# Kernel tuning notes

Hardware: AMD Instinct MI355X
Metric: run time of the kernel (lower is better)

The kernel has to match this reference:

```python
import jax, jax.numpy as jnp
import numpy as np

STEP_SIZE = 0.3333
MAX_STEPS = 8          # >= ceil(max(2*sigma)/step); extra iterations have k==0 (no-op)
TANGENT_DIRECTION = True


def _bilinear_sample(img, p):
    # img: [B,C,H,W], p: [B,2,H,W] normalized coords in [0,1] (x=width, y=height)
    B, C, H, W = img.shape
    fx = p[:, 0] * W - 0.5   # [B,H,W] pixel-center convention
    fy = p[:, 1] * H - 0.5
    x0 = jnp.floor(fx)
    y0 = jnp.floor(fy)
    wx = (fx - x0)[:, None]  # [B,1,H,W]
    wy = (fy - y0)[:, None]
    x0i = jnp.clip(x0.astype(jnp.int32), 0, W - 1)
    x1i = jnp.clip(x0i + 1, 0, W - 1)
    y0i = jnp.clip(y0.astype(jnp.int32), 0, H - 1)
    y1i = jnp.clip(y0i + 1, 0, H - 1)
    gather = jax.vmap(lambda im, yi, xi: im[:, yi, xi])  # per-batch gather -> [B,C,H,W]
    v00 = gather(img, y0i, x0i)
    v01 = gather(img, y0i, x1i)
    v10 = gather(img, y1i, x0i)
    v11 = gather(img, y1i, x1i)
    return (v00 * (1 - wx) + v01 * wx) * (1 - wy) + (v10 * (1 - wx) + v11 * wx) * wy


def _p_start(H, W, dtype):
    xs = (jnp.arange(W, dtype=dtype) + 0.5) / W
    ys = (jnp.arange(H, dtype=dtype) + 0.5) / H
    px = jnp.broadcast_to(xs[None, :], (H, W))
    py = jnp.broadcast_to(ys[:, None], (H, W))
    return jnp.stack([px, py])[None]  # [1,2,H,W]


def _perp(t):
    return jnp.concatenate([t[:, 1:2], -t[:, 0:1]], axis=1)


def _forward(x, tangent, sigma):
    B, C, H, W = x.shape
    dt = x.dtype
    factor = min(H, W) / 1024.0          # input_size_factor relative to 1024 base res
    sigma = sigma * factor               # [B,1,1,1]
    half_width = 2.0 * sigma
    two_sigma2 = 2.0 * sigma * sigma
    step = jnp.asarray(1.0 / (STEP_SIZE * factor), dtype=dt)
    tex = jnp.array([W, H], dtype=dt).reshape(1, 2, 1, 1)
    p0 = _p_start(H, W, dt)

    def one_pass(direction):
        v = direction if TANGENT_DIRECTION else _perp(direction)
        p = p0 + v / tex
        r = jnp.broadcast_to(step, (B, 1, 1, 1))
        c = jnp.zeros_like(x)
        s = jnp.zeros((B, 1, H, W), dt)

        def body(carry, _):
            c, s, v, p, r = carry
            k = jnp.exp(-r * r / two_sigma2)                 # [B,1,1,1]
            k = jnp.where(r < half_width, k, 0.0)
            inb = ((p[:, 0:1] >= 0.0) & (p[:, 0:1] < 1.0) &
                   (p[:, 1:2] >= 0.0) & (p[:, 1:2] < 1.0))   # [B,1,H,W]
            k = jnp.where(inb, k, 0.0)                        # [B,1,H,W]
            c = c + _bilinear_sample(x, p) * k
            s = s + k
            tf = _bilinear_sample(tangent, p)                 # [B,2,H,W]
            if not TANGENT_DIRECTION:
                tf = _perp(tf)
            vt = jnp.sum(v * tf, axis=1, keepdims=True)
            tf = jnp.where(vt < 0.0, -tf, tf)                 # keep marching direction coherent
            return (c, s, tf, p + tf / tex, r + step), None

        (c, s, _, _, _), _ = jax.lax.scan(body, (c, s, v, p, r), None, length=MAX_STEPS)
        return c, s

    c1, s1 = one_pass(tangent)
    c2, s2 = one_pass(-tangent)
    return (x + c1 + c2) / (1.0 + s1 + s2)


def setup_inputs() -> dict:
    key = jax.random.key(0)
    k1, k2, k3 = jax.random.split(key, 3)
    B, C, H, W = 2, 3, 1024, 1024
    x = jax.random.uniform(k1, (B, C, H, W), dtype=jnp.float32)
    t = jax.random.normal(k2, (B, 2, H, W), dtype=jnp.float32)
    t = t / (jnp.sqrt(jnp.sum(t * t, axis=1, keepdims=True)) + 1e-6)  # unit tangent field
    sigma = 2.0 + 4.0 * jax.random.uniform(k3, (B, 1, 1, 1), dtype=jnp.float32)
    return {"x": x, "tangent": t, "sigma": sigma}


def reference(x, tangent, sigma):
    return _forward(x, tangent, sigma)
```

## Files before the change

### kernel.cpp

```cpp
#include <hip/hip_runtime.h>


#define HH 1024
#define WW 1024
#define CC 3
#define BB 2
#define NPIX (HH * WW)

#define TSX 16
#define TSY 16
#define HALO_LO 5
#define NWIN 27

__device__ __forceinline__ unsigned bf16rn(float f) {
    unsigned u = __float_as_uint(f);
    unsigned r = u + 0x7fffu + ((u >> 16) & 1u);
    return r >> 16;
}
__device__ __forceinline__ float bf_lo(unsigned u) { return __uint_as_float(u << 16); }
__device__ __forceinline__ float bf_hi(unsigned u) { return __uint_as_float(u & 0xffff0000u); }

__global__ __launch_bounds__(256) void flow_smooth_lds(
    const float* __restrict__ x, const float* __restrict__ tng,
    const float* __restrict__ sigma, float* __restrict__ out)
{
    __shared__ uint4 win[NWIN * NWIN];

    const int b = blockIdx.z;
    const int tile_x0 = blockIdx.x * TSX;
    const int tile_y0 = blockIdx.y * TSY;
    const int win_x0 = tile_x0 - HALO_LO;
    const int win_y0 = tile_y0 - HALO_LO;

    const float* __restrict__ xb  = x   + (size_t)b * CC * NPIX;
    const float* __restrict__ tbx = tng + (size_t)b * 2 * NPIX;
    const float* __restrict__ tby = tbx + NPIX;

    for (int j = threadIdx.x; j < NWIN * NWIN; j += 256) {
        const int jy = j / NWIN;
        const int jx = j - jy * NWIN;
        const int gy = min(max(win_y0 + jy, 0), HH - 1);
        const int gx = min(max(win_x0 + jx, 0), WW - 1);
        const int g  = gy * WW + gx;
        uint4 rec;
        rec.x = __float_as_uint(tbx[g]);
        rec.y = __float_as_uint(tby[g]);
        rec.z = bf16rn(xb[g]) | (bf16rn(xb[NPIX + g]) << 16);
        rec.w = bf16rn(xb[2 * NPIX + g]);
        win[j] = rec;
    }
    __syncthreads();

    const int ix = tile_x0 + (threadIdx.x & (TSX - 1));
    const int iy = tile_y0 + (threadIdx.x >> 4);
    const int pix = iy * WW + ix;

    const float sig = sigma[b];
    const float half_width = 2.0f * sig;
    const float inv_two_sigma2 = 1.0f / (2.0f * sig * sig);
    const float step = (float)(1.0 / 0.3333);

    const float xc0 = xb[pix];
    const float xc1 = xb[NPIX + pix];
    const float xc2 = xb[2 * NPIX + pix];
    const float t0x = tbx[pix];
    const float t0y = tby[pix];

    const float invW = 1.0f / WW;
    const float invH = 1.0f / HH;

    float acc0 = 0.f, acc1 = 0.f, acc2 = 0.f, accs = 0.f;

    float vx[2], vy[2], px[2], py[2];
    vx[0] = t0x;  vy[0] = t0y;
    vx[1] = -t0x; vy[1] = -t0y;
    const float p0x = ((float)ix + 0.5f) * invW;
    const float p0y = ((float)iy + 0.5f) * invH;
    px[0] = p0x + vx[0] * invW;  py[0] = p0y + vy[0] * invH;
    px[1] = p0x + vx[1] * invW;  py[1] = p0y + vy[1] * invH;

    float r = step;
    for (int it = 0; it < 8; ++it) {
        if (!(r < half_width)) break;
        const float k = __expf(-r * r * inv_two_sigma2);

        #pragma unroll
        for (int c = 0; c < 2; ++c) {
            const float fx = px[c] * (float)WW - 0.5f;
            const float fy = py[c] * (float)HH - 0.5f;
            const float x0f = floorf(fx);
            const float y0f = floorf(fy);
            const float wx = fx - x0f;
            const float wy = fy - y0f;
            int x0i = (int)x0f;
            int y0i = (int)y0f;
            x0i = min(max(x0i, 0), WW - 1);
            y0i = min(max(y0i, 0), HH - 1);
            const int x1i = min(x0i + 1, WW - 1);
            const int y1i = min(y0i + 1, HH - 1);

            const int jx0 = x0i - win_x0;
            const int jx1 = x1i - win_x0;
            const int jy0 = y0i - win_y0;
            const int jy1 = y1i - win_y0;

            const uint4 q00 = win[jy0 * NWIN + jx0];
            const uint4 q01 = win[jy0 * NWIN + jx1];
            const uint4 q10 = win[jy1 * NWIN + jx0];
            const uint4 q11 = win[jy1 * NWIN + jx1];

            const float wxm = 1.f - wx;
            const float wym = 1.f - wy;
            const float w00 = wxm * wym, w01 = wx * wym;
            const float w10 = wxm * wy,  w11 = wx * wy;

            float tfx = __uint_as_float(q00.x) * w00 + __uint_as_float(q01.x) * w01
                      + __uint_as_float(q10.x) * w10 + __uint_as_float(q11.x) * w11;
            float tfy = __uint_as_float(q00.y) * w00 + __uint_as_float(q01.y) * w01
                      + __uint_as_float(q10.y) * w10 + __uint_as_float(q11.y) * w11;

            const bool inb = (px[c] >= 0.f) && (px[c] < 1.f) &&
                             (py[c] >= 0.f) && (py[c] < 1.f);
            if (inb) {
                acc0 += k * (bf_lo(q00.z) * w00 + bf_lo(q01.z) * w01 +
                             bf_lo(q10.z) * w10 + bf_lo(q11.z) * w11);
                acc1 += k * (bf_hi(q00.z) * w00 + bf_hi(q01.z) * w01 +
                             bf_hi(q10.z) * w10 + bf_hi(q11.z) * w11);
                acc2 += k * (bf_lo(q00.w) * w00 + bf_lo(q01.w) * w01 +
                             bf_lo(q10.w) * w10 + bf_lo(q11.w) * w11);
                accs += k;
            }

            const float vt = vx[c] * tfx + vy[c] * tfy;
            if (vt < 0.f) { tfx = -tfx; tfy = -tfy; }
            vx[c] = tfx; vy[c] = tfy;
            px[c] += tfx * invW;
            py[c] += tfy * invH;
        }
        r += step;
    }

    const float inv_den = 1.0f / (1.0f + accs);
    float* ob = out + (size_t)b * CC * NPIX;
    ob[pix]            = (xc0 + acc0) * inv_den;
    ob[NPIX + pix]     = (xc1 + acc1) * inv_den;
    ob[2 * NPIX + pix] = (xc2 + acc2) * inv_den;
}

extern "C" void kernel_launch(void* const* d_in, const int* in_sizes, int n_in,
                              void* d_out, int out_size, void* d_ws, size_t ws_size,
                              hipStream_t stream) {
    const float* x  = (const float*)d_in[0];
    const float* t  = (const float*)d_in[1];
    const float* sg = (const float*)d_in[2];
    float* out = (float*)d_out;

    dim3 grid(WW / TSX, HH / TSY, BB);
    flow_smooth_lds<<<grid, dim3(256), 0, stream>>>(x, t, sg, out);
}
```

Before: 118.7 us.

## Use 32x32 tiles with four pixels per thread and a clamp-free interior path

Result: slower. 123.0 us (+3.6%).

```diff
diff --git a/kernel.cpp b/kernel.cpp
--- a/kernel.cpp
+++ b/kernel.cpp
@@ -1,4 +1,5 @@
 #include <hip/hip_runtime.h>
+#include <hip/hip_fp16.h>
 
 
 #define HH 1024
@@ -7,28 +8,119 @@
 #define BB 2
 #define NPIX (HH * WW)
 
-#define TSX 16
-#define TSY 16
+#define TS 32
 #define HALO_LO 5
-#define NWIN 27
-
-__device__ __forceinline__ unsigned bf16rn(float f) {
-    unsigned u = __float_as_uint(f);
-    unsigned r = u + 0x7fffu + ((u >> 16) & 1u);
-    return r >> 16;
-}
-__device__ __forceinline__ float bf_lo(unsigned u) { return __uint_as_float(u << 16); }
-__device__ __forceinline__ float bf_hi(unsigned u) { return __uint_as_float(u & 0xffff0000u); }
-
-__global__ __launch_bounds__(256) void flow_smooth_lds(
+#define NWIN 43
+#define NREC (NWIN * NWIN)
+
+__device__ __forceinline__ unsigned pk_f16x2(float a, float b) {
+    __half2 h = __floats2half2_rn(a, b);
+    return *(const unsigned*)&h;
+}
+__device__ __forceinline__ float2 unpk_f16x2(unsigned u) {
+    __half2 h = *(const __half2*)&u;
+    return __half22float2(h);
+}
+
+template <bool BORDER>
+__device__ __forceinline__ float4 march_pixel(
+    const uint4* __restrict__ win, int win_x0, int win_y0,
+    int ix, int iy, float t0x, float t0y,
+    float half_width, float inv_two_sigma2, float step)
+{
+    const float invT = 1.0f / 1024.0f;
+    float acc0 = 0.f, acc1 = 0.f, acc2 = 0.f, accs = 0.f;
+
+    float vx[2], vy[2], px[2], py[2];
+    vx[0] = t0x;  vy[0] = t0y;
+    vx[1] = -t0x; vy[1] = -t0y;
+    const float p0x = ((float)ix + 0.5f) * invT;
+    const float p0y = ((float)iy + 0.5f) * invT;
+    px[0] = p0x + vx[0] * invT;  py[0] = p0y + vy[0] * invT;
+    px[1] = p0x + vx[1] * invT;  py[1] = p0y + vy[1] * invT;
+
+    float r = step;
+    for (int it = 0; it < 8; ++it) {
+        if (!(r < half_width)) break;
+        const float k = __expf(-r * r * inv_two_sigma2);
+
+        #pragma unroll
+        for (int c = 0; c < 2; ++c) {
+            const float fx = px[c] * 1024.0f - 0.5f;
+            const float fy = py[c] * 1024.0f - 0.5f;
+            const float x0f = floorf(fx);
+            const float y0f = floorf(fy);
+            const float wx = fx - x0f;
+            const float wy = fy - y0f;
+
+            int jx0, jx1, jy0, jy1;
+            if (BORDER) {
+                int x0i = (int)x0f, y0i = (int)y0f;
+                x0i = min(max(x0i, 0), WW - 1);
+                y0i = min(max(y0i, 0), HH - 1);
+                const int x1i = min(x0i + 1, WW - 1);
+                const int y1i = min(y0i + 1, HH - 1);
+                jx0 = x0i - win_x0; jx1 = x1i - win_x0;
+                jy0 = y0i - win_y0; jy1 = y1i - win_y0;
+            } else {
+                jx0 = (int)x0f - win_x0; jx1 = jx0 + 1;
+                jy0 = (int)y0f - win_y0; jy1 = jy0 + 1;
+            }
+
+            const uint4 q00 = win[jy0 * NWIN + jx0];
+            const uint4 q01 = win[jy0 * NWIN + jx1];
+            const uint4 q10 = win[jy1 * NWIN + jx0];
+            const uint4 q11 = win[jy1 * NWIN + jx1];
+
+            const float wxm = 1.f - wx;
+            const float wym = 1.f - wy;
+            const float w00 = wxm * wym, w01 = wx * wym;
+            const float w10 = wxm * wy,  w11 = wx * wy;
+
+            float tfx = __uint_as_float(q00.x) * w00 + __uint_as_float(q01.x) * w01
+                      + __uint_as_float(q10.x) * w10 + __uint_as_float(q11.x) * w11;
+            float tfy = __uint_as_float(q00.y) * w00 + __uint_as_float(q01.y) * w01
+                      + __uint_as_float(q10.y) * w10 + __uint_as_float(q11.y) * w11;
+
+            bool inb = true;
+            if (BORDER)
+                inb = (px[c] >= 0.f) && (px[c] < 1.f) &&
+                      (py[c] >= 0.f) && (py[c] < 1.f);
+            if (inb) {
+                const float2 a00 = unpk_f16x2(q00.z);
+                const float2 a01 = unpk_f16x2(q01.z);
+                const float2 a10 = unpk_f16x2(q10.z);
+                const float2 a11 = unpk_f16x2(q11.z);
+                const float2 b00 = unpk_f16x2(q00.w);
+                const float2 b01 = unpk_f16x2(q01.w);
+                const float2 b10 = unpk_f16x2(q10.w);
+                const float2 b11 = unpk_f16x2(q11.w);
+                acc0 += k * (a00.x * w00 + a01.x * w01 + a10.x * w10 + a11.x * w11);
+                acc1 += k * (a00.y * w00 + a01.y * w01 + a10.y * w10 + a11.y * w11);
+                acc2 += k * (b00.x * w00 + b01.x * w01 + b10.x * w10 + b11.x * w11);
+                accs += k;
+            }
+
+            const float vt = vx[c] * tfx + vy[c] * tfy;
+            if (vt < 0.f) { tfx = -tfx; tfy = -tfy; }
+            vx[c] = tfx; vy[c] = tfy;
+            px[c] += tfx * invT;
+            py[c] += tfy * invT;
+        }
+        r += step;
+    }
+    return make_float4(acc0, acc1, acc2, accs);
+}
+
+__global__ __launch_bounds__(256) void flow_smooth_lds32(
     const float* __restrict__ x, const float* __restrict__ tng,
     const float* __restrict__ sigma, float* __restrict__ out)
 {
-    __shared__ uint4 win[NWIN * NWIN];
+    __shared__ uint4 win[NREC];
 
     const int b = blockIdx.z;
-    const int tile_x0 = blockIdx.x * TSX;
-    const int tile_y0 = blockIdx.y * TSY;
+    const int tile_x0 = blockIdx.x * TS;
+    const int tile_y0 = blockIdx.y * TS;
     const int win_x0 = tile_x0 - HALO_LO;
     const int win_y0 = tile_y0 - HALO_LO;
 
@@ -36,7 +128,7 @@
     const float* __restrict__ tbx = tng + (size_t)b * 2 * NPIX;
     const float* __restrict__ tby = tbx + NPIX;
 
-    for (int j = threadIdx.x; j < NWIN * NWIN; j += 256) {
+    for (int j = threadIdx.x; j < NREC; j += 256) {
         const int jy = j / NWIN;
         const int jx = j - jy * NWIN;
         const int gy = min(max(win_y0 + jy, 0), HH - 1);
@@ -45,106 +137,65 @@
         uint4 rec;
         rec.x = __float_as_uint(tbx[g]);
         rec.y = __float_as_uint(tby[g]);
-        rec.z = bf16rn(xb[g]) | (bf16rn(xb[NPIX + g]) << 16);
-        rec.w = bf16rn(xb[2 * NPIX + g]);
+        rec.z = pk_f16x2(xb[g], xb[NPIX + g]);
+        rec.w = pk_f16x2(xb[2 * NPIX + g], 0.0f);
         win[j] = rec;
     }
     __syncthreads();
-
-    const int ix = tile_x0 + (threadIdx.x & (TSX - 1));
-    const int iy = tile_y0 + (threadIdx.x >> 4);
-    const int pix = iy * WW + ix;
 
     const float sig = sigma[b];
     const float half_width = 2.0f * sig;
     const float inv_two_sigma2 = 1.0f / (2.0f * sig * sig);
     const float step = (float)(1.0 / 0.3333);
 
-    const float xc0 = xb[pix];
-    const float xc1 = xb[NPIX + pix];
-    const float xc2 = xb[2 * NPIX + pix];
-    const float t0x = tbx[pix];
-    const float t0y = tby[pix];
-
-    const float invW = 1.0f / WW;
-    const float invH = 1.0f / HH;
-
-    float acc0 = 0.f, acc1 = 0.f, acc2 = 0.f, accs = 0.f;
-
-    float vx[2], vy[2], px[2], py[2];
-    vx[0] = t0x;  vy[0] = t0y;
-    vx[1] = -t0x; vy[1] = -t0y;
-    const float p0x = ((float)ix + 0.5f) * invW;
-    const float p0y = ((float)iy + 0.5f) * invH;
-    px[0] = p0x + vx[0] * invW;  py[0] = p0y + vy[0] * invH;
-    px[1] = p0x + vx[1] * invW;  py[1] = p0y + vy[1] * invH;
-
-    float r = step;
-    for (int it = 0; it < 8; ++it) {
-        if (!(r < half_width)) break;
-        const float k = __expf(-r * r * inv_two_sigma2);
-
+    const int tx  = threadIdx.x & 31;
+    const int ty0 = threadIdx.x >> 5;
+    float* __restrict__ ob = out + (size_t)b * CC * NPIX;
+
+    const bool border = (blockIdx.x == 0) | (blockIdx.x == gridDim.x - 1) |
+                        (blockIdx.y == 0) | (blockIdx.y == gridDim.y - 1);
+
+    if (!border) {
         #pragma unroll
-        for (int c = 0; c < 2; ++c) {
-            const float fx = px[c] * (float)WW - 0.5f;
-            const float fy = py[c] * (float)HH - 0.5f;
-            const float x0f = floorf(fx);
-            const float y0f = floorf(fy);
-            const float wx = fx - x0f;
-            const float wy = fy - y0f;
-            int x0i = (int)x0f;
-            int y0i = (int)y0f;
-            x0i = min(max(x0i, 0), WW - 1);
-            y0i = min(max(y0i, 0), HH - 1);
-            const int x1i = min(x0i + 1, WW - 1);
-            const int y1i = min(y0i + 1, HH - 1);
-
-            const int jx0 = x0i - win_x0;
-            const int jx1 = x1i - win_x0;
-            const int jy0 = y0i - win_y0;
-            const int jy1 = y1i - win_y0;
-
-            const uint4 q00 = win[jy0 * NWIN + jx0];
-            const uint4 q01 = win[jy0 * NWIN + jx1];
-            const uint4 q10 = win[jy1 * NWIN + jx0];
-            const uint4 q11 = win[jy1 * NWIN + jx1];
-
-            const float wxm = 1.f - wx;
-            const float wym = 1.f - wy;
-            const float w00 = wxm * wym, w01 = wx * wym;
-            const float w10 = wxm * wy,  w11 = wx * wy;
-
-            float tfx = __uint_as_float(q00.x) * w00 + __uint_as_float(q01.x) * w01
-                      + __uint_as_float(q10.x) * w10 + __uint_as_float(q11.x) * w11;
-            float tfy = __uint_as_float(q00.y) * w00 + __uint_as_float(q01.y) * w01
-                      + __uint_as_float(q10.y) * w10 + __uint_as_float(q11.y) * w11;
-
-            const bool inb = (px[c] >= 0.f) && (px[c] < 1.f) &&
-                             (py[c] >= 0.f) && (py[c] < 1.f);
-            if (inb) {
-                acc0 += k * (bf_lo(q00.z) * w00 + bf_lo(q01.z) * w01 +
-                             bf_lo(q10.z) * w10 + bf_lo(q11.z) * w11);
-                acc1 += k * (bf_hi(q00.z) * w00 + bf_hi(q01.z) * w01 +
-                             bf_hi(q10.z) * w10 + bf_hi(q11.z) * w11);
-                acc2 += k * (bf_lo(q00.w) * w00 + bf_lo(q01.w) * w01 +
-                             bf_lo(q10.w) * w10 + bf_lo(q11.w) * w11);
-                accs += k;
-            }
-
-            const float vt = vx[c] * tfx + vy[c] * tfy;
-            if (vt < 0.f) { tfx = -tfx; tfy = -tfy; }
-            vx[c] = tfx; vy[c] = tfy;
-            px[c] += tfx * invW;
-            py[c] += tfy * invH;
+        for (int q = 0; q < 4; ++q) {
+            const int ly = ty0 + 8 * q;
+            const int ix = tile_x0 + tx;
+            const int iy = tile_y0 + ly;
+            const uint4 own = win[(ly + HALO_LO) * NWIN + (tx + HALO_LO)];
+            const float t0x = __uint_as_float(own.x);
+            const float t0y = __uint_as_float(own.y);
+            const float2 c01 = unpk_f16x2(own.z);
+            const float2 c2p = unpk_f16x2(own.w);
+            const float4 a = march_pixel<false>(win, win_x0, win_y0, ix, iy,
+                                                t0x, t0y, half_width,
+                                                inv_two_sigma2, step);
+            const float inv_den = 1.0f / (1.0f + a.w);
+            const int pix = iy * WW + ix;
+            ob[pix]            = (c01.x + a.x) * inv_den;
+            ob[NPIX + pix]     = (c01.y + a.y) * inv_den;
+            ob[2 * NPIX + pix] = (c2p.x + a.z) * inv_den;
         }
-        r += step;
+    } else {
+        #pragma unroll
+        for (int q = 0; q < 4; ++q) {
+            const int ly = ty0 + 8 * q;
+            const int ix = tile_x0 + tx;
+            const int iy = tile_y0 + ly;
+            const uint4 own = win[(ly + HALO_LO) * NWIN + (tx + HALO_LO)];
+            const float t0x = __uint_as_float(own.x);
+            const float t0y = __uint_as_float(own.y);
+            const float2 c01 = unpk_f16x2(own.z);
+            const float2 c2p = unpk_f16x2(own.w);
+            const float4 a = march_pixel<true>(win, win_x0, win_y0, ix, iy,
+                                               t0x, t0y, half_width,
+                                               inv_two_sigma2, step);
+            const float inv_den = 1.0f / (1.0f + a.w);
+            const int pix = iy * WW + ix;
+            ob[pix]            = (c01.x + a.x) * inv_den;
+            ob[NPIX + pix]     = (c01.y + a.y) * inv_den;
+            ob[2 * NPIX + pix] = (c2p.x + a.z) * inv_den;
+        }
     }
-
-    const float inv_den = 1.0f / (1.0f + accs);
-    float* ob = out + (size_t)b * CC * NPIX;
-    ob[pix]            = (xc0 + acc0) * inv_den;
-    ob[NPIX + pix]     = (xc1 + acc1) * inv_den;
-    ob[2 * NPIX + pix] = (xc2 + acc2) * inv_den;
 }
 
 extern "C" void kernel_launch(void* const* d_in, const int* in_sizes, int n_in,
@@ -155,6 +206,6 @@
     const float* sg = (const float*)d_in[2];
     float* out = (float*)d_out;
 
-    dim3 grid(WW / TSX, HH / TSY, BB);
-    flow_smooth_lds<<<grid, dim3(256), 0, stream>>>(x, t, sg, out);
-}
+    dim3 grid(WW / TS, HH / TS, BB);
+    flow_smooth_lds32<<<grid, dim3(256), 0, stream>>>(x, t, sg, out);
+}
```
